# Performance work log

Hardware: AMD Instinct MI355X
Metric: run time of the kernel (lower is better)

## Reference

```python
import jax, jax.numpy as jnp
import numpy as np

BATCH = 131072
HASHLEN = 64
HID = 180
OUT = 300


def setup_inputs() -> dict:
    key = jax.random.key(0)
    ks = jax.random.split(key, 8)
    scale = 0.05
    return {
        "b": jax.random.normal(ks[0], (BATCH, HASHLEN), dtype=jnp.float32),
        "labels": jax.random.randint(ks[1], (BATCH,), 0, 300),
        "W_h": jax.random.normal(ks[2], (HID, HASHLEN), dtype=jnp.float32) * scale,
        "b_h": jax.random.normal(ks[3], (HID,), dtype=jnp.float32) * scale,
        "W_mu": jax.random.normal(ks[4], (OUT, HID), dtype=jnp.float32) * scale,
        "b_mu": jax.random.normal(ks[5], (OUT,), dtype=jnp.float32) * scale,
        "W_sig": jax.random.normal(ks[6], (OUT, HID), dtype=jnp.float32) * scale,
        "b_sig": jax.random.normal(ks[7], (OUT,), dtype=jnp.float32) * scale,
    }


def reference(b, labels, W_h, b_h, W_mu, b_mu, W_sig, b_sig):
    # h = hidden(b); mean = mu(h); sigma = sigma_layer(h)
    h = b @ W_h.T + b_h                      # [B, 180]
    mean = h @ W_mu.T + b_mu                 # [B, 300]
    sig = h @ W_sig.T + b_sig                # [B, 300]
    # Original builds diag(sig^2) and calls MVN.rsample, which Cholesky-factors
    # the diagonal covariance: L = diag(sqrt(sig^2)) = diag(|sig|).
    # rsample = mean + L @ eps  ==  mean + |sig| * eps  (elementwise).
    std = jnp.abs(sig)
    eps = jax.random.normal(jax.random.key(42), mean.shape, dtype=mean.dtype)
    return mean + std * eps
```

## Files before the change

### kernel.cpp

```cpp
#include <hip/hip_runtime.h>
#include <stdint.h>

#define BATCH   131072
#define HASHLEN 64
#define HID     180
#define OUT     300

#define BM      64
#define NT      256
#define NTILE2  19

#define WH_FRAGS  (12 * 2 * 64)
#define WM_FRAGS  (NTILE2 * 6 * 64)
#define TOT_FRAGS (WH_FRAGS + 2 * WM_FRAGS)
#define WS_NEEDED ((size_t)TOT_FRAGS * 16)

typedef short bf16x8 __attribute__((ext_vector_type(8)));
typedef float f32x4  __attribute__((ext_vector_type(4)));

#define FAST_SQRT(x) __builtin_amdgcn_sqrtf(x)
#define ROTL(x, r) __builtin_amdgcn_alignbit((x), (x), 32u - (r))

__device__ __forceinline__ unsigned threefry_bits(unsigned ctr) {
  const unsigned ks0 = 0u;
  const unsigned ks1 = 42u;
  const unsigned ks2 = 0x1BD11BDAu ^ 0u ^ 42u;
  unsigned x0 = ks0;
  unsigned x1 = ctr + ks1;
#define TF_R(r) { x0 += x1; x1 = ROTL(x1, r); x1 ^= x0; }
  TF_R(13u) TF_R(15u) TF_R(26u) TF_R(6u)
  x0 += ks1; x1 += ks2 + 1u;
  TF_R(17u) TF_R(29u) TF_R(16u) TF_R(24u)
  x0 += ks2; x1 += ks0 + 2u;
  TF_R(13u) TF_R(15u) TF_R(26u) TF_R(6u)
  x0 += ks0; x1 += ks1 + 3u;
  TF_R(17u) TF_R(29u) TF_R(16u) TF_R(24u)
  x0 += ks1; x1 += ks2 + 4u;
  TF_R(13u) TF_R(15u) TF_R(26u) TF_R(6u)
  x0 += ks2; x1 += ks0 + 5u;
#undef TF_R
  return x0 ^ x1;
}

__device__ __forceinline__ float poly_low_sqrt2(float zz) {
  float p = 2.11772e-09f;
  p = fmaf(p, zz, 3.73196e-08f);
  p = fmaf(p, zz, -5.52613e-07f);
  p = fmaf(p, zz, -9.93702e-07f);
  p = fmaf(p, zz, 7.13551e-05f);
  p = fmaf(p, zz, -5.90464e-04f);
  p = fmaf(p, zz, -2.83858e-03f);
  p = fmaf(p, zz, 0.24177160f);
  p = fmaf(p, zz, 2.1233136f);
  return p;
}
__device__ __forceinline__ float poly_high_sqrt2(float v) {
  float p = -6.53600e-05f;
  p = fmaf(p, v, 3.95852e-05f);
  p = fmaf(p, v, 6.35506e-04f);
  p = fmaf(p, v, -2.07827e-03f);
  p = fmaf(p, v, 3.89984e-03f);
  p = fmaf(p, v, -6.22117e-03f);
  p = fmaf(p, v, 9.25254e-03f);
  p = fmaf(p, v, 1.1793807f);
  p = fmaf(p, v, 4.0064340f);
  return p;
}

__device__ __forceinline__ uint16_t f2bf(float f) {
  uint32_t u = __float_as_uint(f);
  return (uint16_t)((u + 0x7FFFu + ((u >> 16) & 1u)) >> 16);
}

__global__ __launch_bounds__(256) void prep_weights(
    const float* __restrict__ W_h, const float* __restrict__ W_mu,
    const float* __restrict__ W_sig, uint16_t* __restrict__ ws)
{
  int f = blockIdx.x * 256 + threadIdx.x;
  if (f >= TOT_FRAGS) return;
  uint16_t vals[8];
  if (f < WH_FRAGS) {
    int nt = f >> 7, s = (f >> 6) & 1, l = f & 63;
    int row = nt * 16 + (l & 15);
    int k0  = s * 32 + (l >> 4) * 8;
#pragma unroll
    for (int j = 0; j < 8; ++j)
      vals[j] = (row < HID) ? f2bf(W_h[row * HASHLEN + k0 + j]) : (uint16_t)0;
  } else {
    int g = f - WH_FRAGS;
    const float* W = (g < WM_FRAGS) ? W_mu : W_sig;
    if (g >= WM_FRAGS) g -= WM_FRAGS;
    int gt = g / 384, s = (g >> 6) % 6, l = g & 63;
    int col = gt * 16 + (l & 15);
    int k0  = s * 32 + (l >> 4) * 8;
#pragma unroll
    for (int j = 0; j < 8; ++j) {
      int k = k0 + j;
      vals[j] = (col < OUT && k < HID) ? f2bf(W[col * HID + k]) : (uint16_t)0;
    }
  }
  uint16_t* dst = ws + (size_t)f * 8;
#pragma unroll
  for (int j = 0; j < 8; ++j) dst[j] = vals[j];
}

__global__ __launch_bounds__(NT, 6) void fused_decoder(
    const float* __restrict__ bin,
    const uint16_t* __restrict__ ws,
    const float* __restrict__ b_h,
    const float* __restrict__ b_mu, const float* __restrict__ b_sig,
    float* __restrict__ out)
{
  __shared__ unsigned char lds[BM * 384];

  const int tid    = threadIdx.x;
  const int l      = tid & 63;
  const int w      = tid >> 6;
  const int lane15 = l & 15;
  const int lhi    = l >> 4;
  const int swzb   = (l & 7) << 4;
  const int row0   = blockIdx.x * BM;
  const int r0     = w * 16;

  const bf16x8* wsWh = (const bf16x8*)ws;
  const bf16x8* wsWm = (const bf16x8*)ws + WH_FRAGS;
  const bf16x8* wsWs = (const bf16x8*)ws + WH_FRAGS + WM_FRAGS;

  {
    const float* brow = bin + (size_t)(row0 + r0 + lane15) * HASHLEN;
    bf16x8 a1[2];
#pragma unroll
    for (int s = 0; s < 2; ++s) {
      float4 v0 = *(const float4*)(brow + s * 32 + lhi * 8);
      float4 v1 = *(const float4*)(brow + s * 32 + lhi * 8 + 4);
      bf16x8 a;
      a[0] = (short)f2bf(v0.x); a[1] = (short)f2bf(v0.y);
      a[2] = (short)f2bf(v0.z); a[3] = (short)f2bf(v0.w);
      a[4] = (short)f2bf(v1.x); a[5] = (short)f2bf(v1.y);
      a[6] = (short)f2bf(v1.z); a[7] = (short)f2bf(v1.w);
      a1[s] = a;
    }
#pragma unroll
    for (int nt = 0; nt < 12; ++nt) {
      f32x4 acc = {0.f, 0.f, 0.f, 0.f};
#pragma unroll
      for (int s = 0; s < 2; ++s)
        acc = __builtin_amdgcn_mfma_f32_16x16x32_bf16(a1[s], wsWh[(nt * 2 + s) * 64 + l], acc, 0, 0, 0);
      int col = nt * 16 + lane15;
      float bias = (col < HID) ? b_h[col] : 0.0f;
#pragma unroll
      for (int q = 0; q < 4; ++q) {
        int row = r0 + lhi * 4 + q;
        float h = (col < HID) ? (acc[q] + bias) : 0.0f;
        *(uint16_t*)(lds + row * 384 + ((2 * col) ^ ((row & 7) << 4))) = f2bf(h);
      }
    }
  }
  __syncthreads();

  bf16x8 a2[6];
#pragma unroll
  for (int s = 0; s < 6; ++s)
    a2[s] = *(const bf16x8*)(lds + (r0 + lane15) * 384 + ((s * 64 + lhi * 16) ^ swzb));

  const uint32_t idx0 = (uint32_t)((row0 + r0 + lhi * 4) * OUT + lane15);

#pragma unroll 1
  for (int gt = 0; gt < NTILE2; ++gt) {
    f32x4 accM = {0.f, 0.f, 0.f, 0.f};
    f32x4 accS = {0.f, 0.f, 0.f, 0.f};
#pragma unroll
    for (int s = 0; s < 6; ++s) {
      accM = __builtin_amdgcn_mfma_f32_16x16x32_bf16(a2[s], wsWm[(gt * 6 + s) * 64 + l], accM, 0, 0, 0);
      accS = __builtin_amdgcn_mfma_f32_16x16x32_bf16(a2[s], wsWs[(gt * 6 + s) * 64 + l], accS, 0, 0, 0);
    }
    const int col = gt * 16 + lane15;
    if (col < OUT) {
      const uint32_t ig = idx0 + (uint32_t)(gt * 16);
      uint32_t bits[4];
#pragma unroll
      for (int q = 0; q < 4; ++q)
        bits[q] = threefry_bits(ig + (uint32_t)(q * OUT));
      float xx[4], z[4], pl[4];
#pragma unroll
      for (int q = 0; q < 4; ++q) {
        float f = __uint_as_float((bits[q] >> 9) | 0x3F800000u) - 1.0f;
        const float LO = -0.99999994f;
        float u = fmaxf(LO, fmaf(f, 2.0f, LO));
        xx[q] = u;
        float t = fmaf(-u, u, 1.0f);
        z[q] = -__log2f(t);
        pl[q] = poly_low_sqrt2(z[q] - 3.6067376f);
      }
#pragma unroll
      for (int q = 0; q < 4; ++q) {
        if (__any(z[q] >= 7.2134752f)) {
          float v = FAST_SQRT(z[q]) - 3.6033669f;
          float ph = poly_high_sqrt2(v);
          pl[q] = (z[q] >= 7.2134752f) ? ph : pl[q];
        }
      }
      const float bmu = b_mu[col];
      const float bsg = b_sig[col];
#pragma unroll
      for (int q = 0; q < 4; ++q) {
        float mu  = accM[q] + bmu;
        float sg  = fabsf(accS[q] + bsg);
        float eps = pl[q] * xx[q];
        out[ig + (uint32_t)(q * OUT)] = fmaf(sg, eps, mu);
      }
    }
  }
}

#define FTILE2  19
#define FCHT    2
#define FNCH    10
#define FSH_OFF   0
#define FSH_BYTES (64 * 384)
#define FU_OFF    FSH_BYTES
#define FSB_OFF   FU_OFF
#define FSWH_OFF  (FU_OFF + 8192)
#define FSWM_OFF  FU_OFF
#define FSWS_OFF  (FU_OFF + 12288)
#define FLDS_BYTES (FSH_BYTES + 32768)

__device__ __forceinline__ float eps_from_bits(uint32_t bits) {
  float f = __uint_as_float((bits >> 9) | 0x3F800000u) - 1.0f;
  const float LO = -0.99999994f;
  float u = fmaxf(LO, fmaf(f, 2.0f, LO));
  float t = fmaf(-u, u, 1.0f);
  float z = -__log2f(t);
  float p = poly_low_sqrt2(z - 3.6067376f);
  if (__any(z >= 7.2134752f)) {
    float ph = poly_high_sqrt2(FAST_SQRT(z) - 3.6033669f);
    p = (z >= 7.2134752f) ? ph : p;
  }
  return p * u;
}

__global__ __launch_bounds__(NT) void fused_decoder_fb(
    const float* __restrict__ bin,
    const float* __restrict__ W_h, const float* __restrict__ b_h,
    const float* __restrict__ W_mu, const float* __restrict__ b_mu,
    const float* __restrict__ W_sig, const float* __restrict__ b_sig,
    float* __restrict__ out)
{
  __shared__ unsigned char lds[FLDS_BYTES];
  const int tid = threadIdx.x;
  const int l = tid & 63, w = tid >> 6;
  const int lane15 = l & 15, lhi = l >> 4;
  const int swzb = (l & 7) << 4;
  const int row0 = blockIdx.x * BM;
  const int r0 = w * 16;
  {
    const float4* src = reinterpret_cast<const float4*>(bin + (size_t)row0 * HASHLEN);
#pragma unroll
    for (int it = 0; it < 4; ++it) {
      int idx = tid + NT * it;
      int r = idx >> 4, k4 = idx & 15;
      float4 v = src[idx];
      uint32_t p0 = f2bf(v.x) | ((uint32_t)f2bf(v.y) << 16);
      uint32_t p1 = f2bf(v.z) | ((uint32_t)f2bf(v.w) << 16);
      int off = FSB_OFF + r * 128 + ((k4 * 8) ^ ((r & 7) << 4));
      *(uint32_t*)(lds + off) = p0;
      *(uint32_t*)(lds + off + 4) = p1;
    }
#pragma unroll
    for (int it = 0; it < 12; ++it) {
      int idx = tid + NT * it;
      int n = idx >> 4, k4 = idx & 15;
      float4 v = make_float4(0.f, 0.f, 0.f, 0.f);
      if (n < HID) v = *(const float4*)(W_h + (size_t)n * HASHLEN + k4 * 4);
      uint32_t p0 = f2bf(v.x) | ((uint32_t)f2bf(v.y) << 16);
      uint32_t p1 = f2bf(v.z) | ((uint32_t)f2bf(v.w) << 16);
      int off = FSWH_OFF + n * 128 + ((k4 * 8) ^ ((n & 7) << 4));
      *(uint32_t*)(lds + off) = p0;
      *(uint32_t*)(lds + off + 4) = p1;
    }
  }
  __syncthreads();
  {
    bf16x8 a1[2];
#pragma unroll
    for (int s = 0; s < 2; ++s)
      a1[s] = *(const bf16x8*)(lds + FSB_OFF + (r0 + lane15) * 128 + ((s * 64 + lhi * 16) ^ swzb));
#pragma unroll
    for (int nt = 0; nt < 12; ++nt) {
      f32x4 acc = {0.f, 0.f, 0.f, 0.f};
#pragma unroll
      for (int s = 0; s < 2; ++s) {
        bf16x8 bf = *(const bf16x8*)(lds + FSWH_OFF + (nt * 16 + lane15) * 128 + ((s * 64 + lhi * 16) ^ swzb));
        acc = __builtin_amdgcn_mfma_f32_16x16x32_bf16(a1[s], bf, acc, 0, 0, 0);
      }
      int col = nt * 16 + lane15;
      float bias = (col < HID) ? b_h[col] : 0.0f;
#pragma unroll
      for (int q = 0; q < 4; ++q) {
        int row = r0 + lhi * 4 + q;
        float h = (col < HID) ? (acc[q] + bias) : 0.0f;
        *(uint16_t*)(lds + FSH_OFF + row * 384 + ((2 * col) ^ ((row & 7) << 4))) = f2bf(h);
      }
    }
  }
  __syncthreads();
  bf16x8 a2[6];
#pragma unroll
  for (int s = 0; s < 6; ++s)
    a2[s] = *(const bf16x8*)(lds + FSH_OFF + (r0 + lane15) * 384 + ((s * 64 + lhi * 16) ^ swzb));
  const int rowi = tid >> 3;
  const int tt8 = tid & 7;
  for (int ch = 0; ch < FNCH; ++ch) {
    const int t0 = ch * FCHT;
    const int ntc = (FTILE2 - t0 < FCHT) ? (FTILE2 - t0) : FCHT;
    if (rowi < ntc * 16) {
      int col = ch * 32 + rowi;
      bool cok = (col < OUT);
      const float* wm = W_mu + (size_t)col * HID;
      const float* wsg = W_sig + (size_t)col * HID;
#pragma unroll
      for (int it = 0; it < 12; ++it) {
        int k2 = tt8 + 8 * it;
        bool kok = cok && (k2 < 90);
        float2 vm = kok ? *(const float2*)(wm + k2 * 2) : make_float2(0.f, 0.f);
        float2 vs = kok ? *(const float2*)(wsg + k2 * 2) : make_float2(0.f, 0.f);
        int off = (k2 * 4) ^ ((rowi & 7) << 4);
        *(uint32_t*)(lds + FSWM_OFF + rowi * 384 + off) = f2bf(vm.x) | ((uint32_t)f2bf(vm.y) << 16);
        *(uint32_t*)(lds + FSWS_OFF + rowi * 384 + off) = f2bf(vs.x) | ((uint32_t)f2bf(vs.y) << 16);
      }
    }
    __syncthreads();
    for (int nt2 = 0; nt2 < ntc; ++nt2) {
      const int gt = t0 + nt2;
      const int crow = nt2 * 16 + lane15;
      f32x4 accM = {0.f, 0.f, 0.f, 0.f};
      f32x4 accS = {0.f, 0.f, 0.f, 0.f};
#pragma unroll
      for (int s = 0; s < 6; ++s) {
        int boff = (s * 64 + lhi * 16) ^ swzb;
        bf16x8 bm = *(const bf16x8*)(lds + FSWM_OFF + crow * 384 + boff);
        bf16x8 bs = *(const bf16x8*)(lds + FSWS_OFF + crow * 384 + boff);
        accM = __builtin_amdgcn_mfma_f32_16x16x32_bf16(a2[s], bm, accM, 0, 0, 0);
        accS = __builtin_amdgcn_mfma_f32_16x16x32_bf16(a2[s], bs, accS, 0, 0, 0);
      }
      const int col = gt * 16 + lane15;
      if (col < OUT) {
        const float bmu = b_mu[col];
        const float bsg = b_sig[col];
#pragma unroll
        for (int q = 0; q < 4; ++q) {
          int row = r0 + lhi * 4 + q;
          int gr = row0 + row;
          float mu = accM[q] + bmu;
          float sg = fabsf(accS[q] + bsg);
          uint32_t gi = (uint32_t)(gr * OUT + col);
          uint32_t bits = threefry_bits(gi);
          float eps = eps_from_bits(bits);
          out[(size_t)gr * OUT + col] = fmaf(sg, eps, mu);
        }
      }
    }
    __syncthreads();
  }
}

extern "C" void kernel_launch(void* const* d_in, const int* in_sizes, int n_in,
                              void* d_out, int out_size, void* d_ws, size_t ws_size,
                              hipStream_t stream) {
  const float* b     = (const float*)d_in[0];
  const float* W_h   = (const float*)d_in[2];
  const float* b_h   = (const float*)d_in[3];
  const float* W_mu  = (const float*)d_in[4];
  const float* b_mu  = (const float*)d_in[5];
  const float* W_sig = (const float*)d_in[6];
  const float* b_sig = (const float*)d_in[7];
  float* out = (float*)d_out;

  if (ws_size >= WS_NEEDED && d_ws != nullptr) {
    uint16_t* ws = (uint16_t*)d_ws;
    hipLaunchKernelGGL(prep_weights, dim3((TOT_FRAGS + 255) / 256), dim3(256), 0, stream,
                       W_h, W_mu, W_sig, ws);
    hipLaunchKernelGGL(fused_decoder, dim3(BATCH / BM), dim3(NT), 0, stream,
                       b, ws, b_h, b_mu, b_sig, out);
  } else {
    hipLaunchKernelGGL(fused_decoder_fb, dim3(BATCH / BM), dim3(NT), 0, stream,
                       b, W_h, b_h, W_mu, b_mu, W_sig, b_sig, out);
  }
}
```

Measured before the change: 148.9 us.

## Process two 16-row tiles per wave to reuse weight fragments across rows

Doubles the rows per block from 64 to 128 so each wave handles 32 rows as two 16-row MFMA tiles. Each loaded weight fragment feeds two MFMAs, halving weight-fragment global loads per output. The cost is more registers (two sets of A operands and four accumulators), more LDS per block, and fewer blocks, with launch bounds lowered to 3 waves per SIMD. The epilogue moves into a helper that runs once per tile.

```diff
diff --git a/kernel.cpp b/kernel.cpp
--- a/kernel.cpp
+++ b/kernel.cpp
@@ -6,7 +6,7 @@
 #define HID     180
 #define OUT     300
 
-#define BM      64
+#define BMM     128
 #define NT      256
 #define NTILE2  19
 
@@ -104,14 +104,50 @@
   for (int j = 0; j < 8; ++j) dst[j] = vals[j];
 }
 
-__global__ __launch_bounds__(NT, 6) void fused_decoder(
+__device__ __forceinline__ void epilogue4(
+    f32x4 accM, f32x4 accS, float bmu, float bsg, uint32_t ig,
+    float* __restrict__ out)
+{
+  uint32_t bits[4];
+#pragma unroll
+  for (int q = 0; q < 4; ++q)
+    bits[q] = threefry_bits(ig + (uint32_t)(q * OUT));
+  float xx[4], z[4], pl[4];
+#pragma unroll
+  for (int q = 0; q < 4; ++q) {
+    float f = __uint_as_float((bits[q] >> 9) | 0x3F800000u) - 1.0f;
+    const float LO = -0.99999994f;
+    float u = fmaxf(LO, fmaf(f, 2.0f, LO));
+    xx[q] = u;
+    float t = fmaf(-u, u, 1.0f);
+    z[q] = -__log2f(t);
+    pl[q] = poly_low_sqrt2(z[q] - 3.6067376f);
+  }
+#pragma unroll
+  for (int q = 0; q < 4; ++q) {
+    if (__any(z[q] >= 7.2134752f)) {
+      float v = FAST_SQRT(z[q]) - 3.6033669f;
+      float ph = poly_high_sqrt2(v);
+      pl[q] = (z[q] >= 7.2134752f) ? ph : pl[q];
+    }
+  }
+#pragma unroll
+  for (int q = 0; q < 4; ++q) {
+    float mu  = accM[q] + bmu;
+    float sg  = fabsf(accS[q] + bsg);
+    float eps = pl[q] * xx[q];
+    out[ig + (uint32_t)(q * OUT)] = fmaf(sg, eps, mu);
+  }
+}
+
+__global__ __launch_bounds__(NT, 3) void fused_decoder(
     const float* __restrict__ bin,
     const uint16_t* __restrict__ ws,
     const float* __restrict__ b_h,
     const float* __restrict__ b_mu, const float* __restrict__ b_sig,
     float* __restrict__ out)
 {
-  __shared__ unsigned char lds[BM * 384];
+  __shared__ unsigned char lds[BMM * 384];
 
   const int tid    = threadIdx.x;
   const int l      = tid & 63;
@@ -119,100 +155,96 @@
   const int lane15 = l & 15;
   const int lhi    = l >> 4;
   const int swzb   = (l & 7) << 4;
-  const int row0   = blockIdx.x * BM;
-  const int r0     = w * 16;
+  const int row0   = blockIdx.x * BMM;
+  const int r0     = w * 32;
 
   const bf16x8* wsWh = (const bf16x8*)ws;
   const bf16x8* wsWm = (const bf16x8*)ws + WH_FRAGS;
   const bf16x8* wsWs = (const bf16x8*)ws + WH_FRAGS + WM_FRAGS;
 
   {
-    const float* brow = bin + (size_t)(row0 + r0 + lane15) * HASHLEN;
-    bf16x8 a1[2];
-#pragma unroll
-    for (int s = 0; s < 2; ++s) {
-      float4 v0 = *(const float4*)(brow + s * 32 + lhi * 8);
-      float4 v1 = *(const float4*)(brow + s * 32 + lhi * 8 + 4);
-      bf16x8 a;
-      a[0] = (short)f2bf(v0.x); a[1] = (short)f2bf(v0.y);
-      a[2] = (short)f2bf(v0.z); a[3] = (short)f2bf(v0.w);
-      a[4] = (short)f2bf(v1.x); a[5] = (short)f2bf(v1.y);
-      a[6] = (short)f2bf(v1.z); a[7] = (short)f2bf(v1.w);
-      a1[s] = a;
+    bf16x8 a1[2][2];
+#pragma unroll
+    for (int t = 0; t < 2; ++t) {
+      const float* brow = bin + (size_t)(row0 + r0 + t * 16 + lane15) * HASHLEN;
+#pragma unroll
+      for (int s = 0; s < 2; ++s) {
+        float4 v0 = *(const float4*)(brow + s * 32 + lhi * 8);
+        float4 v1 = *(const float4*)(brow + s * 32 + lhi * 8 + 4);
+        bf16x8 a;
+        a[0] = (short)f2bf(v0.x); a[1] = (short)f2bf(v0.y);
+        a[2] = (short)f2bf(v0.z); a[3] = (short)f2bf(v0.w);
+        a[4] = (short)f2bf(v1.x); a[5] = (short)f2bf(v1.y);
+        a[6] = (short)f2bf(v1.z); a[7] = (short)f2bf(v1.w);
+        a1[t][s] = a;
+      }
     }
 #pragma unroll
     for (int nt = 0; nt < 12; ++nt) {
-      f32x4 acc = {0.f, 0.f, 0.f, 0.f};
-#pragma unroll
-      for (int s = 0; s < 2; ++s)
-        acc = __builtin_amdgcn_mfma_f32_16x16x32_bf16(a1[s], wsWh[(nt * 2 + s) * 64 + l], acc, 0, 0, 0);
+      f32x4 acc0 = {0.f, 0.f, 0.f, 0.f};
+      f32x4 acc1 = {0.f, 0.f, 0.f, 0.f};
+#pragma unroll
+      for (int s = 0; s < 2; ++s) {
+        bf16x8 bw = wsWh[(nt * 2 + s) * 64 + l];
+        acc0 = __builtin_amdgcn_mfma_f32_16x16x32_bf16(a1[0][s], bw, acc0, 0, 0, 0);
+        acc1 = __builtin_amdgcn_mfma_f32_16x16x32_bf16(a1[1][s], bw, acc1, 0, 0, 0);
+      }
       int col = nt * 16 + lane15;
       float bias = (col < HID) ? b_h[col] : 0.0f;
 #pragma unroll
       for (int q = 0; q < 4; ++q) {
-        int row = r0 + lhi * 4 + q;
-        float h = (col < HID) ? (acc[q] + bias) : 0.0f;
-        *(uint16_t*)(lds + row * 384 + ((2 * col) ^ ((row & 7) << 4))) = f2bf(h);
+        int row0t = r0 + lhi * 4 + q;
+        float h0 = (col < HID) ? (acc0[q] + bias) : 0.0f;
+        *(uint16_t*)(lds + row0t * 384 + ((2 * col) ^ ((row0t & 7) << 4))) = f2bf(h0);
+        int row1t = row0t + 16;
+        float h1 = (col < HID) ? (acc1[q] + bias) : 0.0f;
+        *(uint16_t*)(lds + row1t * 384 + ((2 * col) ^ ((row1t & 7) << 4))) = f2bf(h1);
       }
     }
   }
   __syncthreads();
 
-  bf16x8 a2[6];
-#pragma unroll
-  for (int s = 0; s < 6; ++s)
-    a2[s] = *(const bf16x8*)(lds + (r0 + lane15) * 384 + ((s * 64 + lhi * 16) ^ swzb));
-
-  const uint32_t idx0 = (uint32_t)((row0 + r0 + lhi * 4) * OUT + lane15);
+  bf16x8 a2l[6], a2h[6];
+#pragma unroll
+  for (int s = 0; s < 6; ++s) {
+    int boff = (s * 64 + lhi * 16) ^ swzb;
+    a2l[s] = *(const bf16x8*)(lds + (r0 + lane15) * 384 + boff);
+    a2h[s] = *(const bf16x8*)(lds + (r0 + 16 + lane15) * 384 + boff);
+  }
+
+  const uint32_t ig_l = (uint32_t)((row0 + r0 + lhi * 4) * OUT + lane15);
+  const uint32_t ig_h = ig_l + (uint32_t)(16 * OUT);
 
 #pragma unroll 1
   for (int gt = 0; gt < NTILE2; ++gt) {
-    f32x4 accM = {0.f, 0.f, 0.f, 0.f};
-    f32x4 accS = {0.f, 0.f, 0.f, 0.f};
+    f32x4 aMl = {0.f, 0.f, 0.f, 0.f};
+    f32x4 aMh = {0.f, 0.f, 0.f, 0.f};
+    f32x4 aSl = {0.f, 0.f, 0.f, 0.f};
+    f32x4 aSh = {0.f, 0.f, 0.f, 0.f};
 #pragma unroll
     for (int s = 0; s < 6; ++s) {
-      accM = __builtin_amdgcn_mfma_f32_16x16x32_bf16(a2[s], wsWm[(gt * 6 + s) * 64 + l], accM, 0, 0, 0);
-      accS = __builtin_amdgcn_mfma_f32_16x16x32_bf16(a2[s], wsWs[(gt * 6 + s) * 64 + l], accS, 0, 0, 0);
+      bf16x8 bm = wsWm[(gt * 6 + s) * 64 + l];
+      aMl = __builtin_amdgcn_mfma_f32_16x16x32_bf16(a2l[s], bm, aMl, 0, 0, 0);
+      aMh = __builtin_amdgcn_mfma_f32_16x16x32_bf16(a2h[s], bm, aMh, 0, 0, 0);
+    }
+#pragma unroll
+    for (int s = 0; s < 6; ++s) {
+      bf16x8 bs2 = wsWs[(gt * 6 + s) * 64 + l];
+      aSl = __builtin_amdgcn_mfma_f32_16x16x32_bf16(a2l[s], bs2, aSl, 0, 0, 0);
+      aSh = __builtin_amdgcn_mfma_f32_16x16x32_bf16(a2h[s], bs2, aSh, 0, 0, 0);
     }
     const int col = gt * 16 + lane15;
     if (col < OUT) {
-      const uint32_t ig = idx0 + (uint32_t)(gt * 16);
-      uint32_t bits[4];
-#pragma unroll
-      for (int q = 0; q < 4; ++q)
-        bits[q] = threefry_bits(ig + (uint32_t)(q * OUT));
-      float xx[4], z[4], pl[4];
-#pragma unroll
-      for (int q = 0; q < 4; ++q) {
-        float f = __uint_as_float((bits[q] >> 9) | 0x3F800000u) - 1.0f;
-        const float LO = -0.99999994f;
-        float u = fmaxf(LO, fmaf(f, 2.0f, LO));
-        xx[q] = u;
-        float t = fmaf(-u, u, 1.0f);
-        z[q] = -__log2f(t);
-        pl[q] = poly_low_sqrt2(z[q] - 3.6067376f);
-      }
-#pragma unroll
-      for (int q = 0; q < 4; ++q) {
-        if (__any(z[q] >= 7.2134752f)) {
-          float v = FAST_SQRT(z[q]) - 3.6033669f;
-          float ph = poly_high_sqrt2(v);
-          pl[q] = (z[q] >= 7.2134752f) ? ph : pl[q];
-        }
-      }
       const float bmu = b_mu[col];
       const float bsg = b_sig[col];
-#pragma unroll
-      for (int q = 0; q < 4; ++q) {
-        float mu  = accM[q] + bmu;
-        float sg  = fabsf(accS[q] + bsg);
-        float eps = pl[q] * xx[q];
-        out[ig + (uint32_t)(q * OUT)] = fmaf(sg, eps, mu);
-      }
-    }
-  }
-}
-
+      const uint32_t go = (uint32_t)(gt * 16);
+      epilogue4(aMl, aSl, bmu, bsg, ig_l + go, out);
+      epilogue4(aMh, aSh, bmu, bsg, ig_h + go, out);
+    }
+  }
+}
+
+#define FBM     64
 #define FTILE2  19
 #define FCHT    2
 #define FNCH    10
@@ -251,7 +283,7 @@
   const int l = tid & 63, w = tid >> 6;
   const int lane15 = l & 15, lhi = l >> 4;
   const int swzb = (l & 7) << 4;
-  const int row0 = blockIdx.x * BM;
+  const int row0 = blockIdx.x * FBM;
   const int r0 = w * 16;
   {
     const float4* src = reinterpret_cast<const float4*>(bin + (size_t)row0 * HASHLEN);
@@ -380,10 +412,10 @@
     uint16_t* ws = (uint16_t*)d_ws;
     hipLaunchKernelGGL(prep_weights, dim3((TOT_FRAGS + 255) / 256), dim3(256), 0, stream,
                        W_h, W_mu, W_sig, ws);
-    hipLaunchKernelGGL(fused_decoder, dim3(BATCH / BM), dim3(NT), 0, stream,
+    hipLaunchKernelGGL(fused_decoder, dim3(BATCH / BMM), dim3(NT), 0, stream,
                        b, ws, b_h, b_mu, b_sig, out);
   } else {
-    hipLaunchKernelGGL(fused_decoder_fb, dim3(BATCH / BM), dim3(NT), 0, stream,
+    hipLaunchKernelGGL(fused_decoder_fb, dim3(BATCH / FBM), dim3(NT), 0, stream,
                        b, W_h, b_h, W_mu, b_mu, W_sig, b_sig, out);
   }
 }
```

Result: slower. 161.3 us (+8.3%).

## Swap MFMA operand order to transpose outputs for vectorized stores

Applied to the files above, without the earlier changes.

Swaps the A/B operands of the MFMA calls so each lane's accumulator holds four consecutive output columns of one row instead of four rows of one column. This lets the hidden-layer result go to LDS as packed 8-byte writes, lets biases load as float4, and lets the final output be written with one 16-byte store per lane instead of four scattered scalar stores. The last partial tile is peeled so the main loop has no column bound check. The __syncthreads between the LDS write and read is removed on the assumption that each wave reads only its own 16 rows, which relies on same-wave LDS ordering.

```diff
diff --git a/kernel.cpp b/kernel.cpp
--- a/kernel.cpp
+++ b/kernel.cpp
@@ -104,6 +104,43 @@
   for (int j = 0; j < 8; ++j) dst[j] = vals[j];
 }
 
+__device__ __forceinline__ void epilogue4(
+    f32x4 accM, f32x4 accS, f32x4 bm4, f32x4 bs4, uint32_t gi0,
+    float* __restrict__ out)
+{
+  uint32_t bits[4];
+#pragma unroll
+  for (int q = 0; q < 4; ++q)
+    bits[q] = threefry_bits(gi0 + (uint32_t)q);
+  float xx[4], z[4], pl[4];
+#pragma unroll
+  for (int q = 0; q < 4; ++q) {
+    float f = __uint_as_float((bits[q] >> 9) | 0x3F800000u) - 1.0f;
+    const float LO = -0.99999994f;
+    float u = fmaxf(LO, fmaf(f, 2.0f, LO));
+    xx[q] = u;
+    float t = fmaf(-u, u, 1.0f);
+    z[q] = -__log2f(t);
+    pl[q] = poly_low_sqrt2(z[q] - 3.6067376f);
+  }
+#pragma unroll
+  for (int q = 0; q < 4; ++q) {
+    if (__any(z[q] >= 7.2134752f)) {
+      float v = FAST_SQRT(z[q]) - 3.6033669f;
+      float ph = poly_high_sqrt2(v);
+      pl[q] = (z[q] >= 7.2134752f) ? ph : pl[q];
+    }
+  }
+  f32x4 res;
+#pragma unroll
+  for (int q = 0; q < 4; ++q) {
+    float mu  = accM[q] + bm4[q];
+    float sg  = fabsf(accS[q] + bs4[q]);
+    res[q] = fmaf(sg, pl[q] * xx[q], mu);
+  }
+  *(f32x4*)(out + gi0) = res;
+}
+
 __global__ __launch_bounds__(NT, 6) void fused_decoder(
     const float* __restrict__ bin,
     const uint16_t* __restrict__ ws,
@@ -118,7 +155,7 @@
   const int w      = tid >> 6;
   const int lane15 = l & 15;
   const int lhi    = l >> 4;
-  const int swzb   = (l & 7) << 4;
+  const int swzb   = (lane15 & 7) << 4;
   const int row0   = blockIdx.x * BM;
   const int r0     = w * 16;
 
@@ -128,7 +165,7 @@
 
   {
     const float* brow = bin + (size_t)(row0 + r0 + lane15) * HASHLEN;
-    bf16x8 a1[2];
+    bf16x8 bfrag[2];
 #pragma unroll
     for (int s = 0; s < 2; ++s) {
       float4 v0 = *(const float4*)(brow + s * 32 + lhi * 8);
@@ -138,77 +175,67 @@
       a[2] = (short)f2bf(v0.z); a[3] = (short)f2bf(v0.w);
       a[4] = (short)f2bf(v1.x); a[5] = (short)f2bf(v1.y);
       a[6] = (short)f2bf(v1.z); a[7] = (short)f2bf(v1.w);
-      a1[s] = a;
-    }
+      bfrag[s] = a;
+    }
+    const int row = r0 + lane15;
 #pragma unroll
     for (int nt = 0; nt < 12; ++nt) {
       f32x4 acc = {0.f, 0.f, 0.f, 0.f};
 #pragma unroll
       for (int s = 0; s < 2; ++s)
-        acc = __builtin_amdgcn_mfma_f32_16x16x32_bf16(a1[s], wsWh[(nt * 2 + s) * 64 + l], acc, 0, 0, 0);
-      int col = nt * 16 + lane15;
-      float bias = (col < HID) ? b_h[col] : 0.0f;
-#pragma unroll
-      for (int q = 0; q < 4; ++q) {
-        int row = r0 + lhi * 4 + q;
-        float h = (col < HID) ? (acc[q] + bias) : 0.0f;
-        *(uint16_t*)(lds + row * 384 + ((2 * col) ^ ((row & 7) << 4))) = f2bf(h);
-      }
-    }
-  }
-  __syncthreads();
+        acc = __builtin_amdgcn_mfma_f32_16x16x32_bf16(wsWh[(nt * 2 + s) * 64 + l], bfrag[s], acc, 0, 0, 0);
+      const int k0 = nt * 16 + lhi * 4;
+      f32x4 bias = {0.f, 0.f, 0.f, 0.f};
+      if (k0 <= HID - 4) bias = *(const f32x4*)(b_h + k0);
+      const bool ok = (k0 < HID);
+      float h0 = ok ? (acc[0] + bias[0]) : 0.0f;
+      float h1 = ok ? (acc[1] + bias[1]) : 0.0f;
+      float h2 = ok ? (acc[2] + bias[2]) : 0.0f;
+      float h3 = ok ? (acc[3] + bias[3]) : 0.0f;
+      uint2 pk;
+      pk.x = (uint32_t)f2bf(h0) | ((uint32_t)f2bf(h1) << 16);
+      pk.y = (uint32_t)f2bf(h2) | ((uint32_t)f2bf(h3) << 16);
+      *(uint2*)(lds + row * 384 + ((2 * k0) ^ swzb)) = pk;
+    }
+  }
 
   bf16x8 a2[6];
 #pragma unroll
   for (int s = 0; s < 6; ++s)
     a2[s] = *(const bf16x8*)(lds + (r0 + lane15) * 384 + ((s * 64 + lhi * 16) ^ swzb));
 
-  const uint32_t idx0 = (uint32_t)((row0 + r0 + lhi * 4) * OUT + lane15);
+  const uint32_t idx0 = (uint32_t)((row0 + r0 + lane15) * OUT + lhi * 4);
 
 #pragma unroll 1
-  for (int gt = 0; gt < NTILE2; ++gt) {
+  for (int gt = 0; gt < NTILE2 - 1; ++gt) {
     f32x4 accM = {0.f, 0.f, 0.f, 0.f};
     f32x4 accS = {0.f, 0.f, 0.f, 0.f};
 #pragma unroll
+    for (int s = 0; s < 6; ++s)
+      accM = __builtin_amdgcn_mfma_f32_16x16x32_bf16(wsWm[(gt * 6 + s) * 64 + l], a2[s], accM, 0, 0, 0);
+#pragma unroll
+    for (int s = 0; s < 6; ++s)
+      accS = __builtin_amdgcn_mfma_f32_16x16x32_bf16(wsWs[(gt * 6 + s) * 64 + l], a2[s], accS, 0, 0, 0);
+    const int c0 = gt * 16 + lhi * 4;
+    f32x4 bm4 = *(const f32x4*)(b_mu + c0);
+    f32x4 bs4 = *(const f32x4*)(b_sig + c0);
+    epilogue4(accM, accS, bm4, bs4, idx0 + (uint32_t)(gt * 16), out);
+  }
+
+  {
+    const int gt = NTILE2 - 1;
+    f32x4 accM = {0.f, 0.f, 0.f, 0.f};
+    f32x4 accS = {0.f, 0.f, 0.f, 0.f};
+#pragma unroll
     for (int s = 0; s < 6; ++s) {
-      accM = __builtin_amdgcn_mfma_f32_16x16x32_bf16(a2[s], wsWm[(gt * 6 + s) * 64 + l], accM, 0, 0, 0);
-      accS = __builtin_amdgcn_mfma_f32_16x16x32_bf16(a2[s], wsWs[(gt * 6 + s) * 64 + l], accS, 0, 0, 0);
-    }
-    const int col = gt * 16 + lane15;
-    if (col < OUT) {
-      const uint32_t ig = idx0 + (uint32_t)(gt * 16);
-      uint32_t bits[4];
-#pragma unroll
-      for (int q = 0; q < 4; ++q)
-        bits[q] = threefry_bits(ig + (uint32_t)(q * OUT));
-      float xx[4], z[4], pl[4];
-#pragma unroll
-      for (int q = 0; q < 4; ++q) {
-        float f = __uint_as_float((bits[q] >> 9) | 0x3F800000u) - 1.0f;
-        const float LO = -0.99999994f;
-        float u = fmaxf(LO, fmaf(f, 2.0f, LO));
-        xx[q] = u;
-        float t = fmaf(-u, u, 1.0f);
-        z[q] = -__log2f(t);
-        pl[q] = poly_low_sqrt2(z[q] - 3.6067376f);
-      }
-#pragma unroll
-      for (int q = 0; q < 4; ++q) {
-        if (__any(z[q] >= 7.2134752f)) {
-          float v = FAST_SQRT(z[q]) - 3.6033669f;
-          float ph = poly_high_sqrt2(v);
-          pl[q] = (z[q] >= 7.2134752f) ? ph : pl[q];
-        }
-      }
-      const float bmu = b_mu[col];
-      const float bsg = b_sig[col];
-#pragma unroll
-      for (int q = 0; q < 4; ++q) {
-        float mu  = accM[q] + bmu;
-        float sg  = fabsf(accS[q] + bsg);
-        float eps = pl[q] * xx[q];
-        out[ig + (uint32_t)(q * OUT)] = fmaf(sg, eps, mu);
-      }
+      accM = __builtin_amdgcn_mfma_f32_16x16x32_bf16(wsWm[(gt * 6 + s) * 64 + l], a2[s], accM, 0, 0, 0);
+      accS = __builtin_amdgcn_mfma_f32_16x16x32_bf16(wsWs[(gt * 6 + s) * 64 + l], a2[s], accS, 0, 0, 0);
+    }
+    if (lhi < 3) {
+      const int c0 = gt * 16 + lhi * 4;
+      f32x4 bm4 = *(const f32x4*)(b_mu + c0);
+      f32x4 bs4 = *(const f32x4*)(b_sig + c0);
+      epilogue4(accM, accS, bm4, bs4, idx0 + (uint32_t)(gt * 16), out);
     }
   }
 }
```

Measured after the change: 145.3 us. 1.02x faster.
